# Kernel optimization log

Hardware: AMD Instinct MI355X
Metric: run time of the kernel (lower is better)

The kernel has to match this reference:

```python
import jax, jax.numpy as jnp
import numpy as np

E = 2048   # embedding_size
H = 16     # n_heads
D = E // H # head_dimension = 128
B = 4
N = 2048


def setup_inputs() -> dict:
    key = jax.random.key(0)
    ks = jax.random.split(key, 5)
    scale_qkv = 1.0 / np.sqrt(E)
    scale_fc = 1.0 / np.sqrt(E)
    return {
        "x": jax.random.normal(ks[0], (B, N, E), dtype=jnp.float32),
        # torch Linear(E, E + 2*D); stored as [in, out] for x @ W
        "w_qkv": jax.random.uniform(ks[1], (E, E + 2 * D), jnp.float32, -scale_qkv, scale_qkv),
        "b_qkv": jax.random.uniform(ks[2], (E + 2 * D,), jnp.float32, -scale_qkv, scale_qkv),
        "w_fc": jax.random.uniform(ks[3], (E, E), jnp.float32, -scale_fc, scale_fc),
        "b_fc": jax.random.uniform(ks[4], (E,), jnp.float32, -scale_fc, scale_fc),
    }


def reference(x, w_qkv, b_qkv, w_fc, b_fc):
    b, n, _ = x.shape
    qkv = x @ w_qkv + b_qkv                         # [B,N,E+2D]
    q = qkv[..., :E].reshape(b, n, H, D)            # [B,N,H,D]
    k = qkv[..., E:E + D]                           # [B,N,D] single KV head (MQA)
    v = qkv[..., E + D:]                            # [B,N,D]
    # scores: queries per head against shared keys
    scores = jnp.einsum("bnhd,bmd->bhnm", q, k) / jnp.sqrt(jnp.float32(D))
    # causal mask: triu(ones, diagonal=1) positions filled with -inf
    causal = jnp.triu(jnp.ones((n, n), dtype=bool), k=1)
    scores = jnp.where(causal, -jnp.inf, scores)
    attn = jax.nn.softmax(scores, axis=-1)          # [B,H,N,N]
    out = jnp.einsum("bhnm,bmd->bnhd", attn, v)     # [B,N,H,D]
    out = out.reshape(b, n, E)
    return out @ w_fc + b_fc                        # dropout=0 (eval): identity
```

## Files before the change

kernel.cpp:

```cpp
#include <hip/hip_runtime.h>

#define E_DIM 2048
#define H_NUM 16
#define D_HEAD 128
#define B_SZ 4
#define N_SEQ 2048
#define QKV_LD 2304
#define MROWS_T (B_SZ * N_SEQ)
#define PLS 40
#define SC2F 0.12751744802582937f

typedef __attribute__((ext_vector_type(8))) __bf16 bfx8;
typedef __attribute__((ext_vector_type(8))) short sx8;
typedef __attribute__((ext_vector_type(4))) short sx4;
typedef __attribute__((ext_vector_type(2))) short sx2;
typedef __attribute__((ext_vector_type(4))) float fx4;

__device__ __forceinline__ fx4 mfma_bf16(bfx8 a, bfx8 b, fx4 c) {
    return __builtin_amdgcn_mfma_f32_16x16x32_bf16(a, b, c, 0, 0, 0);
}

__device__ __forceinline__ short f2bf(float f) {
    unsigned u = __builtin_bit_cast(unsigned, f);
    u += 0x7FFFu + ((u >> 16) & 1u);
    return (short)(u >> 16);
}

__device__ __forceinline__ int cvt_pk_bf16(float a, float b) {
    int r;
    asm("v_cvt_pk_bf16_f32 %0, %1, %2" : "=v"(r) : "v"(a), "v"(b));
    return r;
}

__device__ __forceinline__ void gld_lds16(const void* g, void* l) {
    __builtin_amdgcn_global_load_lds((__attribute__((address_space(1))) void*)(void*)g,
                                     (__attribute__((address_space(3))) void*)l, 16, 0, 0);
}

__global__ __launch_bounds__(256) void cast_f32_bf16(const float* __restrict__ in,
                                                     short* __restrict__ out, int n) {
    int i = (blockIdx.x * 256 + threadIdx.x) * 4;
    if (i >= n) return;
    float4 v = *(const float4*)(in + i);
    sx4 r = {f2bf(v.x), f2bf(v.y), f2bf(v.z), f2bf(v.w)};
    *(sx4*)(out + i) = r;
}

__global__ __launch_bounds__(256) void transpose_cast(const float* __restrict__ in,
                                                      short* __restrict__ out, int R, int C) {
    __shared__ float tile[32][33];
    int c0 = blockIdx.x * 32, r0 = blockIdx.y * 32;
    int tx = threadIdx.x;
    for (int i = threadIdx.y; i < 32; i += 8)
        tile[i][tx] = in[(size_t)(r0 + i) * C + c0 + tx];
    __syncthreads();
    for (int i = threadIdx.y; i < 32; i += 8)
        out[(size_t)(c0 + i) * R + r0 + tx] = f2bf(tile[tx][i]);
}

__global__ __launch_bounds__(256) void v_transpose(const short* __restrict__ qkv,
                                                   short* __restrict__ vtg) {
    __shared__ short tile[32][33];
    int r0 = blockIdx.x * 32;
    int d0 = blockIdx.y * 32;
    int tx = threadIdx.x;
    for (int i = threadIdx.y; i < 32; i += 8)
        tile[i][tx] = qkv[(size_t)(r0 + i) * QKV_LD + (E_DIM + D_HEAD) + d0 + tx];
    __syncthreads();
    int kp = ((tx & 15) << 1) | (tx >> 4);
    for (int i = threadIdx.y; i < 32; i += 8)
        vtg[(size_t)(d0 + i) * MROWS_T + r0 + kp] = tile[tx][i];
}

template <bool OUT_BF16, bool SCALE_Q>
__global__ __launch_bounds__(256) void gemm_bt(const short* __restrict__ A,
                                               const short* __restrict__ Bt,
                                               const float* __restrict__ bias,
                                               void* __restrict__ Cp,
                                               int M, int N, int ldc, int K) {
    __shared__ __align__(16) short As[128 * 32];
    __shared__ __align__(16) short Bs[128 * 32];
    const int tid = threadIdx.x, wave = tid >> 6, lane = tid & 63;
    const int quad = lane >> 4, l16 = lane & 15;

    const int gx = gridDim.x;
    int wg = blockIdx.y * gx + blockIdx.x;
    {
        const int nwg = gx * gridDim.y;
        const int qd = nwg >> 3, rm = nwg & 7;
        const int xcd = wg & 7, loc = wg >> 3;
        wg = (xcd < rm ? xcd * (qd + 1) : rm * (qd + 1) + (xcd - rm) * qd) + loc;
    }
    const int m0 = (wg / gx) * 128, n0 = (wg % gx) * 128;

    const int wm = (wave >> 1) * 64, wn = (wave & 1) * 64;
    const int srow = lane >> 2, scol = (lane & 3) * 8;

    fx4 acc[4][4];
#pragma unroll
    for (int mt = 0; mt < 4; ++mt)
#pragma unroll
        for (int nt = 0; nt < 4; ++nt) acc[mt][nt] = (fx4){0.f, 0.f, 0.f, 0.f};

    const short* Ag = A + (size_t)m0 * K;
    const short* Bg = Bt + (size_t)n0 * K;

    for (int k0 = 0; k0 < K; k0 += 32) {
#pragma unroll
        for (int i = 0; i < 2; ++i) {
            int chunk = wave * 2 + i;
            int row = chunk * 16 + srow;
            gld_lds16(Ag + (size_t)row * K + k0 + scol, &As[chunk * 512]);
            gld_lds16(Bg + (size_t)row * K + k0 + scol, &Bs[chunk * 512]);
        }
        __syncthreads();
        bfx8 af[4], bfr[4];
#pragma unroll
        for (int t = 0; t < 4; ++t) {
            af[t]  = *(const bfx8*)&As[(wm + t * 16 + l16) * 32 + quad * 8];
            bfr[t] = *(const bfx8*)&Bs[(wn + t * 16 + l16) * 32 + quad * 8];
        }
#pragma unroll
        for (int mt = 0; mt < 4; ++mt)
#pragma unroll
            for (int nt = 0; nt < 4; ++nt)
                acc[mt][nt] = mfma_bf16(af[mt], bfr[nt], acc[mt][nt]);
        __syncthreads();
    }

    const float scl = (SCALE_Q && n0 < E_DIM) ? SC2F : 1.0f;
    float bv[4];
#pragma unroll
    for (int nt = 0; nt < 4; ++nt) bv[nt] = bias[n0 + wn + nt * 16 + l16];

#pragma unroll
    for (int mt = 0; mt < 4; ++mt)
#pragma unroll
        for (int nt = 0; nt < 4; ++nt)
#pragma unroll
            for (int j = 0; j < 4; ++j) {
                int row = m0 + wm + mt * 16 + quad * 4 + j;
                int col = n0 + wn + nt * 16 + l16;
                float v = (acc[mt][nt][j] + bv[nt]) * scl;
                if (OUT_BF16)
                    ((short*)Cp)[(size_t)row * ldc + col] = f2bf(v);
                else
                    ((float*)Cp)[(size_t)row * ldc + col] = v;
            }
}

template <bool OUT_BF16, bool SCALE_ALL>
__global__ __launch_bounds__(512) void gemm256(const short* __restrict__ A,
                                               const short* __restrict__ Bt,
                                               const float* __restrict__ bias,
                                               void* __restrict__ Cp,
                                               int M, int N, int ldc, int K) {
    __shared__ __align__(16) short lds[2][2][2][8192];
    const int tid = threadIdx.x, wave = tid >> 6, lane = tid & 63;
    const int quad = lane >> 4, l16 = lane & 15;
    const int wmi = wave >> 2, wni = wave & 3;
    const int m0 = blockIdx.y * 256, n0 = blockIdx.x * 256;

    const size_t rstep = (size_t)128 * K;
    const int srow = wave * 16 + (lane >> 2);
    const int sslot = (lane & 3) ^ ((lane >> 3) & 3);
    const short* Asrc = A + ((size_t)(m0 + srow)) * K + sslot * 8;
    const short* Bsrc = Bt + ((size_t)(n0 + srow)) * K + sslot * 8;

    auto stage = [&](const short* srcb, short* dstb, int kcol0) {
        gld_lds16(srcb + kcol0, dstb + wave * 512);
        gld_lds16(srcb + kcol0 + rstep, dstb + 4096 + wave * 512);
    };

    const int swl = (l16 >> 1) & 3;
    const int aoff = (wmi * 128 + l16) * 32 + (quad ^ swl) * 8;
    const int boff = (wni * 64 + l16) * 32 + (quad ^ swl) * 8;

    fx4 acc[8][4];
#pragma unroll
    for (int m = 0; m < 8; ++m)
#pragma unroll
        for (int n = 0; n < 4; ++n) acc[m][n] = (fx4){0.f, 0.f, 0.f, 0.f};

    const int nt = K >> 6;

    stage(Asrc, &lds[0][0][0][0], 0);
    stage(Bsrc, &lds[0][0][1][0], 0);
    stage(Asrc, &lds[0][1][0][0], 32);
    stage(Bsrc, &lds[0][1][1][0], 32);
    stage(Asrc, &lds[1][0][0][0], 64);
    stage(Bsrc, &lds[1][0][1][0], 64);
    asm volatile("s_waitcnt vmcnt(4)");
    __builtin_amdgcn_s_barrier();
    __builtin_amdgcn_sched_barrier(0);

#pragma unroll 1
    for (int t = 0; t < nt; ++t) {
        const int cur = t & 1, nxt = cur ^ 1;
        const short* Ah0 = &lds[cur][0][0][0];
        const short* Bh0 = &lds[cur][0][1][0];
        const short* Ah1 = &lds[cur][1][0][0];
        const short* Bh1 = &lds[cur][1][1][0];
        const int kc = t * 64;
        bfx8 af[4], bf0[4], bf1[4];

#pragma unroll
        for (int n = 0; n < 4; ++n) bf0[n] = *(const bfx8*)&Bh0[boff + n * 512];
#pragma unroll
        for (int m = 0; m < 4; ++m) af[m] = *(const bfx8*)&Ah0[aoff + m * 512];
        if (t + 1 < nt) stage(Asrc, &lds[nxt][1][0][0], kc + 96);
        __builtin_amdgcn_s_barrier();
        __builtin_amdgcn_sched_barrier(0);
        __builtin_amdgcn_s_setprio(1);
#pragma unroll
        for (int m = 0; m < 4; ++m)
#pragma unroll
            for (int n = 0; n < 4; ++n) acc[m][n] = mfma_bf16(af[m], bf0[n], acc[m][n]);
        __builtin_amdgcn_s_setprio(0);
        __builtin_amdgcn_s_barrier();
        __builtin_amdgcn_sched_barrier(0);

#pragma unroll
        for (int m = 0; m < 4; ++m) af[m] = *(const bfx8*)&Ah0[aoff + (m + 4) * 512];
        if (t + 1 < nt) stage(Bsrc, &lds[nxt][1][1][0], kc + 96);
        __builtin_amdgcn_s_barrier();
        __builtin_amdgcn_sched_barrier(0);
        __builtin_amdgcn_s_setprio(1);
#pragma unroll
        for (int m = 0; m < 4; ++m)
#pragma unroll
            for (int n = 0; n < 4; ++n) acc[m + 4][n] = mfma_bf16(af[m], bf0[n], acc[m + 4][n]);
        __builtin_amdgcn_s_setprio(0);
        __builtin_amdgcn_s_barrier();
        __builtin_amdgcn_sched_barrier(0);

#pragma unroll
        for (int n = 0; n < 4; ++n) bf1[n] = *(const bfx8*)&Bh1[boff + n * 512];
#pragma unroll
        for (int m = 0; m < 4; ++m) af[m] = *(const bfx8*)&Ah1[aoff + m * 512];
        if (t + 2 < nt) stage(Asrc, &lds[cur][0][0][0], kc + 128);
        __builtin_amdgcn_s_barrier();
        __builtin_amdgcn_sched_barrier(0);
        __builtin_amdgcn_s_setprio(1);
#pragma unroll
        for (int m = 0; m < 4; ++m)
#pragma unroll
            for (int n = 0; n < 4; ++n) acc[m][n] = mfma_bf16(af[m], bf1[n], acc[m][n]);
        __builtin_amdgcn_s_setprio(0);
        __builtin_amdgcn_s_barrier();
        __builtin_amdgcn_sched_barrier(0);

#pragma unroll
        for (int m = 0; m < 4; ++m) af[m] = *(const bfx8*)&Ah1[aoff + (m + 4) * 512];
        if (t + 2 < nt) stage(Bsrc, &lds[cur][0][1][0], kc + 128);
        __builtin_amdgcn_s_barrier();
        __builtin_amdgcn_sched_barrier(0);
        __builtin_amdgcn_s_setprio(1);
#pragma unroll
        for (int m = 0; m < 4; ++m)
#pragma unroll
            for (int n = 0; n < 4; ++n) acc[m + 4][n] = mfma_bf16(af[m], bf1[n], acc[m + 4][n]);
        __builtin_amdgcn_s_setprio(0);
        if (t < nt - 2) asm volatile("s_waitcnt vmcnt(4)");
        else            asm volatile("s_waitcnt vmcnt(0)");
        __builtin_amdgcn_s_barrier();
        __builtin_amdgcn_sched_barrier(0);
    }

    const float scl = SCALE_ALL ? SC2F : 1.0f;
    float bvn[4];
#pragma unroll
    for (int n = 0; n < 4; ++n) bvn[n] = bias[n0 + wni * 64 + n * 16 + l16];

#pragma unroll
    for (int m = 0; m < 8; ++m)
#pragma unroll
        for (int n = 0; n < 4; ++n)
#pragma unroll
            for (int j = 0; j < 4; ++j) {
                int row = m0 + wmi * 128 + m * 16 + quad * 4 + j;
                int col = n0 + wni * 64 + n * 16 + l16;
                float v = (acc[m][n][j] + bvn[n]) * scl;
                if (OUT_BF16)
                    ((short*)Cp)[(size_t)row * ldc + col] = f2bf(v);
                else
                    ((float*)Cp)[(size_t)row * ldc + col] = v;
            }
}

__global__ __launch_bounds__(256, 2) void attn_kernel(const short* __restrict__ qkv,
                                                      const short* __restrict__ vtg,
                                                      short* __restrict__ outp) {
    __shared__ __align__(16) short Ks[2][4096];
    __shared__ __align__(16) short Vt[2][4096];
    __shared__ __align__(16) short pl[4 * 32 * PLS];
    const int b = blockIdx.y >> 4, h = blockIdx.y & 15;
    const int tid = threadIdx.x, wave = tid >> 6, lane = tid & 63;
    const int quad = lane >> 4, l16 = lane & 15;
    const size_t baseRow = (size_t)b * N_SEQ;
    short* plw = pl + wave * 32 * PLS;

    const int sl = lane ^ ((lane >> 3) & 7);
    const int srow = sl >> 2, sq = sl & 3;
    const int rslot = ((l16 * 4 + quad) ^ ((l16 >> 1) & 7)) * 8;

    auto stage = [&](int k0, int bufi) {
#pragma unroll
        for (int i = 0; i < 2; ++i) {
            const int c = wave * 2 + i;
            gld_lds16(qkv + (baseRow + k0 + (c & 1) * 16 + srow) * QKV_LD + E_DIM +
                          (c >> 1) * 32 + sq * 8,
                      &Ks[bufi][c * 512]);
            gld_lds16(vtg + (size_t)(c * 16 + srow) * MROWS_T + baseRow + k0 + sq * 8,
                      &Vt[bufi][c * 512]);
        }
    };

#pragma unroll 1
    for (int half = 0; half < 2; ++half) {
        const int chunk = half ? (15 - blockIdx.x) : blockIdx.x;
        const int q0 = chunk * 128;
        const int wrow = q0 + wave * 32;

        bfx8 aq0[4], aq1[4];
        {
            const short* qb0 = qkv + (baseRow + wrow + l16) * QKV_LD + h * D_HEAD + quad * 8;
            const short* qb1 = qb0 + 16 * QKV_LD;
#pragma unroll
            for (int c = 0; c < 4; ++c) {
                aq0[c] = *(const bfx8*)(qb0 + c * 32);
                aq1[c] = *(const bfx8*)(qb1 + c * 32);
            }
        }

        fx4 accO0[8], accO1[8];
        float l0[4], l1[4];
#pragma unroll
        for (int dt = 0; dt < 8; ++dt) {
            accO0[dt] = (fx4){0.f, 0.f, 0.f, 0.f};
            accO1[dt] = (fx4){0.f, 0.f, 0.f, 0.f};
        }
#pragma unroll
        for (int j = 0; j < 4; ++j) { l0[j] = 0.f; l1[j] = 0.f; }

        const int nbulk = 4 * chunk;
        const int nkt = nbulk + 4;

        __syncthreads();
        stage(0, 0);

#pragma unroll 1
        for (int kt = 0; kt < nkt; ++kt) {
            __syncthreads();
            if (kt + 1 < nkt) stage((kt + 1) << 5, (kt + 1) & 1);
            const short* ks = Ks[kt & 1];
            const short* vs = Vt[kt & 1];
            const int k0 = kt << 5;

            fx4 s00 = {0.f, 0.f, 0.f, 0.f}, s01 = {0.f, 0.f, 0.f, 0.f};
            fx4 s10 = {0.f, 0.f, 0.f, 0.f}, s11 = {0.f, 0.f, 0.f, 0.f};
            __builtin_amdgcn_s_setprio(1);
#pragma unroll
            for (int dc = 0; dc < 4; ++dc) {
                bfx8 kf0 = *(const bfx8*)&ks[(dc * 2 + 0) * 512 + rslot];
                bfx8 kf1 = *(const bfx8*)&ks[(dc * 2 + 1) * 512 + rslot];
                s00 = mfma_bf16(aq0[dc], kf0, s00);
                s01 = mfma_bf16(aq0[dc], kf1, s01);
                s10 = mfma_bf16(aq1[dc], kf0, s10);
                s11 = mfma_bf16(aq1[dc], kf1, s11);
            }
            __builtin_amdgcn_s_setprio(0);

            bfx8 bvr[8];
#pragma unroll
            for (int dt = 0; dt < 8; ++dt)
                bvr[dt] = *(const bfx8*)&vs[dt * 512 + rslot];

            const bool diag = kt >= nbulk;
#pragma unroll
            for (int j = 0; j < 4; ++j) {
                float e0 = __builtin_amdgcn_exp2f(s00[j]);
                float e1 = __builtin_amdgcn_exp2f(s01[j]);
                if (diag) {
                    const int rb = wrow + quad * 4 + j;
                    e0 = (k0 + l16 <= rb) ? e0 : 0.f;
                    e1 = (k0 + 16 + l16 <= rb) ? e1 : 0.f;
                }
                l0[j] += e0 + e1;
                int pk = cvt_pk_bf16(e0, e1);
                *(sx2*)&plw[(quad * 4 + j) * PLS + 2 * l16] = __builtin_bit_cast(sx2, pk);
            }
#pragma unroll
            for (int j = 0; j < 4; ++j) {
                float e0 = __builtin_amdgcn_exp2f(s10[j]);
                float e1 = __builtin_amdgcn_exp2f(s11[j]);
                if (diag) {
                    const int rb = wrow + 16 + quad * 4 + j;
                    e0 = (k0 + l16 <= rb) ? e0 : 0.f;
                    e1 = (k0 + 16 + l16 <= rb) ? e1 : 0.f;
                }
                l1[j] += e0 + e1;
                int pk = cvt_pk_bf16(e0, e1);
                *(sx2*)&plw[(16 + quad * 4 + j) * PLS + 2 * l16] = __builtin_bit_cast(sx2, pk);
            }

            sx8 aps0 = *(const sx8*)&plw[l16 * PLS + quad * 8];
            sx8 aps1 = *(const sx8*)&plw[(16 + l16) * PLS + quad * 8];
            bfx8 ap0 = __builtin_bit_cast(bfx8, aps0);
            bfx8 ap1 = __builtin_bit_cast(bfx8, aps1);
            __builtin_amdgcn_s_setprio(1);
#pragma unroll
            for (int dt = 0; dt < 8; ++dt) {
                accO0[dt] = mfma_bf16(ap0, bvr[dt], accO0[dt]);
                accO1[dt] = mfma_bf16(ap1, bvr[dt], accO1[dt]);
            }
            __builtin_amdgcn_s_setprio(0);
        }

#pragma unroll
        for (int off = 1; off < 16; off <<= 1)
#pragma unroll
            for (int j = 0; j < 4; ++j) {
                l0[j] += __shfl_xor(l0[j], off);
                l1[j] += __shfl_xor(l1[j], off);
            }
#pragma unroll
        for (int j = 0; j < 4; ++j) {
            float rl0 = 1.0f / l0[j];
            float rl1 = 1.0f / l1[j];
            size_t ob0 = (baseRow + wrow + quad * 4 + j) * (size_t)E_DIM + h * D_HEAD + l16;
            size_t ob1 = ob0 + (size_t)16 * E_DIM;
#pragma unroll
            for (int dt = 0; dt < 8; ++dt) {
                outp[ob0 + dt * 16] = f2bf(accO0[dt][j] * rl0);
                outp[ob1 + dt * 16] = f2bf(accO1[dt][j] * rl1);
            }
        }
    }
}

extern "C" void kernel_launch(void* const* d_in, const int* in_sizes, int n_in,
                              void* d_out, int out_size, void* d_ws, size_t ws_size,
                              hipStream_t stream) {
    const float* x     = (const float*)d_in[0];
    const float* w_qkv = (const float*)d_in[1];
    const float* b_qkv = (const float*)d_in[2];
    const float* w_fc  = (const float*)d_in[3];
    const float* b_fc  = (const float*)d_in[4];
    float* out = (float*)d_out;

    const size_t MROWS = (size_t)B_SZ * N_SEQ;
    short* xb    = (short*)d_ws;
    short* wqkvt = xb + MROWS * E_DIM;
    short* wfct  = wqkvt + (size_t)QKV_LD * E_DIM;
    short* qkvb  = wfct + (size_t)E_DIM * E_DIM;
    short* attnb = qkvb + MROWS * QKV_LD;
    short* vtg   = xb;

    cast_f32_bf16<<<dim3((int)(MROWS * E_DIM / 1024)), dim3(256), 0, stream>>>(
        x, xb, (int)(MROWS * E_DIM));
    transpose_cast<<<dim3(QKV_LD / 32, E_DIM / 32), dim3(32, 8), 0, stream>>>(
        w_qkv, wqkvt, E_DIM, QKV_LD);
    transpose_cast<<<dim3(E_DIM / 32, E_DIM / 32), dim3(32, 8), 0, stream>>>(
        w_fc, wfct, E_DIM, E_DIM);

    gemm256<true, true><<<dim3(E_DIM / 256, (int)(MROWS / 256)), dim3(512), 0, stream>>>(
        xb, wqkvt, b_qkv, qkvb, (int)MROWS, E_DIM, QKV_LD, E_DIM);
    gemm_bt<true, false><<<dim3(2, (int)(MROWS / 128)), dim3(256), 0, stream>>>(
        xb, wqkvt + (size_t)E_DIM * E_DIM, b_qkv + E_DIM, qkvb + E_DIM,
        (int)MROWS, 2 * D_HEAD, QKV_LD, E_DIM);

    v_transpose<<<dim3(MROWS_T / 32, D_HEAD / 32), dim3(32, 8), 0, stream>>>(qkvb, vtg);

    attn_kernel<<<dim3(8, B_SZ * H_NUM), dim3(256), 0, stream>>>(qkvb, vtg, attnb);

    gemm256<false, false><<<dim3(E_DIM / 256, (int)(MROWS / 256)), dim3(512), 0, stream>>>(
        attnb, wfct, b_fc, out, (int)MROWS, E_DIM, E_DIM, E_DIM);
}
```

Baseline: 437.5 us.

## Compute transposed scores so P stays in registers, dropping LDS round-trip

Swaps the MFMA operand order for the QK^T product so each lane holds scores for one query row across consecutive keys. The packed bf16 probabilities can then be fed straight into the PV MFMA as the A operand, with no write to and read back from shared memory. The row-sum bookkeeping shrinks to one scalar per lane, reduced with cross-quad shuffles and redistributed by shuffle at the end. This removes per-iteration LDS stores and loads and the wave-local sync they imply, and frees LDS, in exchange for reworked causal-mask indexing that must exactly match the MFMA output layout.

```diff
diff --git a/kernel.cpp b/kernel.cpp
--- a/kernel.cpp
+++ b/kernel.cpp
@@ -7,13 +7,13 @@
 #define N_SEQ 2048
 #define QKV_LD 2304
 #define MROWS_T (B_SZ * N_SEQ)
-#define PLS 40
 #define SC2F 0.12751744802582937f
 
 typedef __attribute__((ext_vector_type(8))) __bf16 bfx8;
 typedef __attribute__((ext_vector_type(8))) short sx8;
 typedef __attribute__((ext_vector_type(4))) short sx4;
 typedef __attribute__((ext_vector_type(2))) short sx2;
+typedef __attribute__((ext_vector_type(4))) int ix4;
 typedef __attribute__((ext_vector_type(4))) float fx4;
 
 __device__ __forceinline__ fx4 mfma_bf16(bfx8 a, bfx8 b, fx4 c) {
@@ -293,12 +293,10 @@
                                                       short* __restrict__ outp) {
     __shared__ __align__(16) short Ks[2][4096];
     __shared__ __align__(16) short Vt[2][4096];
-    __shared__ __align__(16) short pl[4 * 32 * PLS];
     const int b = blockIdx.y >> 4, h = blockIdx.y & 15;
     const int tid = threadIdx.x, wave = tid >> 6, lane = tid & 63;
     const int quad = lane >> 4, l16 = lane & 15;
     const size_t baseRow = (size_t)b * N_SEQ;
-    short* plw = pl + wave * 32 * PLS;
 
     const int sl = lane ^ ((lane >> 3) & 7);
     const int srow = sl >> 2, sq = sl & 3;
@@ -334,14 +332,12 @@
         }
 
         fx4 accO0[8], accO1[8];
-        float l0[4], l1[4];
+        float l0 = 0.f, l1 = 0.f;
 #pragma unroll
         for (int dt = 0; dt < 8; ++dt) {
             accO0[dt] = (fx4){0.f, 0.f, 0.f, 0.f};
             accO1[dt] = (fx4){0.f, 0.f, 0.f, 0.f};
         }
-#pragma unroll
-        for (int j = 0; j < 4; ++j) { l0[j] = 0.f; l1[j] = 0.f; }
 
         const int nbulk = 4 * chunk;
         const int nkt = nbulk + 4;
@@ -364,10 +360,10 @@
             for (int dc = 0; dc < 4; ++dc) {
                 bfx8 kf0 = *(const bfx8*)&ks[(dc * 2 + 0) * 512 + rslot];
                 bfx8 kf1 = *(const bfx8*)&ks[(dc * 2 + 1) * 512 + rslot];
-                s00 = mfma_bf16(aq0[dc], kf0, s00);
-                s01 = mfma_bf16(aq0[dc], kf1, s01);
-                s10 = mfma_bf16(aq1[dc], kf0, s10);
-                s11 = mfma_bf16(aq1[dc], kf1, s11);
+                s00 = mfma_bf16(kf0, aq0[dc], s00);
+                s01 = mfma_bf16(kf1, aq0[dc], s01);
+                s10 = mfma_bf16(kf0, aq1[dc], s10);
+                s11 = mfma_bf16(kf1, aq1[dc], s11);
             }
             __builtin_amdgcn_s_setprio(0);
 
@@ -377,37 +373,36 @@
                 bvr[dt] = *(const bfx8*)&vs[dt * 512 + rslot];
 
             const bool diag = kt >= nbulk;
+            int pk0[4], pk1[4];
 #pragma unroll
             for (int j = 0; j < 4; ++j) {
                 float e0 = __builtin_amdgcn_exp2f(s00[j]);
                 float e1 = __builtin_amdgcn_exp2f(s01[j]);
                 if (diag) {
-                    const int rb = wrow + quad * 4 + j;
-                    e0 = (k0 + l16 <= rb) ? e0 : 0.f;
-                    e1 = (k0 + 16 + l16 <= rb) ? e1 : 0.f;
+                    const int key = k0 + quad * 4 + j;
+                    const int qr = wrow + l16;
+                    e0 = (key <= qr) ? e0 : 0.f;
+                    e1 = (key + 16 <= qr) ? e1 : 0.f;
                 }
-                l0[j] += e0 + e1;
-                int pk = cvt_pk_bf16(e0, e1);
-                *(sx2*)&plw[(quad * 4 + j) * PLS + 2 * l16] = __builtin_bit_cast(sx2, pk);
+                l0 += e0 + e1;
+                pk0[j] = cvt_pk_bf16(e0, e1);
             }
 #pragma unroll
             for (int j = 0; j < 4; ++j) {
                 float e0 = __builtin_amdgcn_exp2f(s10[j]);
                 float e1 = __builtin_amdgcn_exp2f(s11[j]);
                 if (diag) {
-                    const int rb = wrow + 16 + quad * 4 + j;
-                    e0 = (k0 + l16 <= rb) ? e0 : 0.f;
-                    e1 = (k0 + 16 + l16 <= rb) ? e1 : 0.f;
+                    const int key = k0 + quad * 4 + j;
+                    const int qr = wrow + 16 + l16;
+                    e0 = (key <= qr) ? e0 : 0.f;
+                    e1 = (key + 16 <= qr) ? e1 : 0.f;
                 }
-                l1[j] += e0 + e1;
-                int pk = cvt_pk_bf16(e0, e1);
-                *(sx2*)&plw[(16 + quad * 4 + j) * PLS + 2 * l16] = __builtin_bit_cast(sx2, pk);
-            }
-
-            sx8 aps0 = *(const sx8*)&plw[l16 * PLS + quad * 8];
-            sx8 aps1 = *(const sx8*)&plw[(16 + l16) * PLS + quad * 8];
-            bfx8 ap0 = __builtin_bit_cast(bfx8, aps0);
-            bfx8 ap1 = __builtin_bit_cast(bfx8, aps1);
+                l1 += e0 + e1;
+                pk1[j] = cvt_pk_bf16(e0, e1);
+            }
+
+            bfx8 ap0 = __builtin_bit_cast(bfx8, (ix4){pk0[0], pk0[1], pk0[2], pk0[3]});
+            bfx8 ap1 = __builtin_bit_cast(bfx8, (ix4){pk1[0], pk1[1], pk1[2], pk1[3]});
             __builtin_amdgcn_s_setprio(1);
 #pragma unroll
             for (int dt = 0; dt < 8; ++dt) {
@@ -417,17 +412,13 @@
             __builtin_amdgcn_s_setprio(0);
         }
 
-#pragma unroll
-        for (int off = 1; off < 16; off <<= 1)
-#pragma unroll
-            for (int j = 0; j < 4; ++j) {
-                l0[j] += __shfl_xor(l0[j], off);
-                l1[j] += __shfl_xor(l1[j], off);
-            }
+        l0 += __shfl_xor(l0, 16); l0 += __shfl_xor(l0, 32);
+        l1 += __shfl_xor(l1, 16); l1 += __shfl_xor(l1, 32);
+
 #pragma unroll
         for (int j = 0; j < 4; ++j) {
-            float rl0 = 1.0f / l0[j];
-            float rl1 = 1.0f / l1[j];
+            float rl0 = 1.0f / __shfl(l0, quad * 4 + j);
+            float rl1 = 1.0f / __shfl(l1, quad * 4 + j);
             size_t ob0 = (baseRow + wrow + quad * 4 + j) * (size_t)E_DIM + h * D_HEAD + l16;
             size_t ob1 = ob0 + (size_t)16 * E_DIM;
 #pragma unroll
```

After: 422.2 us. 1.04x faster.
